# Kernel tuning notes

Measured on AMD Instinct MI355X. Metric: run time of the kernel, lower is better.

The kernel has to match this reference:

```python
import jax, jax.numpy as jnp
import numpy as np

ALPHA = 0.9
EPS = 1e-5
SEQ, BATCH, D_MODEL, FF_DIM = 2048, 16, 512, 2048


def _layer_norm(x, g, b):
    m = jnp.mean(x, axis=-1, keepdims=True)
    v = jnp.mean((x - m) ** 2, axis=-1, keepdims=True)
    return (x - m) * jax.lax.rsqrt(v + EPS) * g + b


def _decay_matrix(seq, dtype):
    # Closed form of the torch roll/flip/tril loop:
    #   W[i, j] = alpha^{i-j+1}            for j <= i
    #   W[i, i] += 1 - sum_{k=1}^{i+1} alpha^k   (diag correction)
    i = jnp.arange(seq)
    diff = i[:, None] - i[None, :]                       # [S, S]
    causal = diff >= 0
    expo = jnp.where(causal, diff + 1, 0).astype(dtype)
    W = jnp.where(causal, jnp.asarray(ALPHA, dtype) ** expo, 0.0)
    W = W + jnp.diag(1.0 - W.sum(axis=1))
    return W


def setup_inputs() -> dict:
    key = jax.random.key(0)
    ks = jax.random.split(key, 8)
    s = lambda fan: 1.0 / np.sqrt(fan)
    return {
        "x": jax.random.normal(ks[0], (SEQ, BATCH, D_MODEL), jnp.float32),
        "w_lin": jax.random.normal(ks[1], (D_MODEL, D_MODEL), jnp.float32) * s(D_MODEL),
        "b_lin": jax.random.normal(ks[2], (D_MODEL,), jnp.float32) * 0.01,
        "w1": jax.random.normal(ks[3], (FF_DIM, D_MODEL), jnp.float32) * s(D_MODEL),
        "b1": jax.random.normal(ks[4], (FF_DIM,), jnp.float32) * 0.01,
        "w2": jax.random.normal(ks[5], (D_MODEL, FF_DIM), jnp.float32) * s(FF_DIM),
        "b2": jax.random.normal(ks[6], (D_MODEL,), jnp.float32) * 0.01,
        "g1": jnp.ones((D_MODEL,), jnp.float32),
        "beta1": jnp.zeros((D_MODEL,), jnp.float32),
        "g2": jnp.ones((D_MODEL,), jnp.float32),
        "beta2": jnp.zeros((D_MODEL,), jnp.float32),
    }


def reference(x, w_lin, b_lin, w1, b1, w2, b2, g1, beta1, g2, beta2):
    seq = x.shape[0]
    W = _decay_matrix(seq, x.dtype)                      # [S, S]

    # attention sublayer (dropout = identity in eval)
    y = _layer_norm(x, g1, beta1)
    z = jnp.einsum("sbd,ed->sbe", y, w_lin) + b_lin       # projection
    attn = jnp.einsum("ih,hbd->ibd", W, z)                # causal exp-decay mixing
    x = x + attn

    # feed-forward sublayer
    y = _layer_norm(x, g2, beta2)
    h = jax.nn.relu(jnp.einsum("sbd,fd->sbf", y, w1) + b1)
    ff = jnp.einsum("sbf,df->sbd", h, w2) + b2
    return x + ff
```

## Files before the change

kernel.cpp:

```cpp
#include <hip/hip_runtime.h>

#define SEQ 2048
#define BATCH 16
#define DMODEL 512
#define FFDIM 2048
#define NTOK (SEQ * BATCH)
#define ALPHA 0.9f

typedef unsigned short u16;
typedef unsigned int u32;
typedef __attribute__((ext_vector_type(8))) short short8;
typedef __attribute__((ext_vector_type(4))) float f32x4;

__device__ __forceinline__ float bf2f(u16 u) {
    unsigned int v = ((unsigned int)u) << 16;
    return __builtin_bit_cast(float, v);
}
__device__ __forceinline__ u16 f2bf(float f) {
    unsigned int v = __builtin_bit_cast(unsigned int, f);
    v += 0x7fffu + ((v >> 16) & 1u);
    return (u16)(v >> 16);
}

__global__ __launch_bounds__(256) void cvt_kernel(const float* __restrict__ in,
                                                  u16* __restrict__ out, int n) {
    const int i = (blockIdx.x * 256 + threadIdx.x) * 4;
    if (i >= n) return;
    float4 v = *(const float4*)(in + i);
    ushort4 o;
    o.x = f2bf(v.x); o.y = f2bf(v.y); o.z = f2bf(v.z); o.w = f2bf(v.w);
    *(ushort4*)(out + i) = o;
}

__global__ __launch_bounds__(256) void ln_kernel(const float* __restrict__ xin,
                                                 const float* __restrict__ g,
                                                 const float* __restrict__ b,
                                                 u16* __restrict__ y) {
    const int lane = threadIdx.x & 63;
    const int wave = threadIdx.x >> 6;
    const long tok = (long)blockIdx.x * 4 + wave;
    const long off = tok * DMODEL + lane * 8;

    float f[8];
    {
        const float4* xp = (const float4*)(xin + off);
        float4 a = xp[0], c = xp[1];
        f[0] = a.x; f[1] = a.y; f[2] = a.z; f[3] = a.w;
        f[4] = c.x; f[5] = c.y; f[6] = c.z; f[7] = c.w;
    }
    float s = 0.f, s2 = 0.f;
#pragma unroll
    for (int i = 0; i < 8; i++) { s += f[i]; s2 += f[i] * f[i]; }
#pragma unroll
    for (int o = 32; o > 0; o >>= 1) {
        s += __shfl_xor(s, o, 64);
        s2 += __shfl_xor(s2, o, 64);
    }
    const float mean = s * (1.f / DMODEL);
    const float var = s2 * (1.f / DMODEL) - mean * mean;
    const float inv = rsqrtf(var + 1e-5f);

    const float4* gp = (const float4*)(g + lane * 8);
    const float4* bp = (const float4*)(b + lane * 8);
    float4 g0 = gp[0], g1 = gp[1], b0 = bp[0], b1 = bp[1];
    float gg[8] = {g0.x, g0.y, g0.z, g0.w, g1.x, g1.y, g1.z, g1.w};
    float bb[8] = {b0.x, b0.y, b0.z, b0.w, b1.x, b1.y, b1.z, b1.w};
    short8 ov;
#pragma unroll
    for (int i = 0; i < 8; i++)
        ov[i] = (short)f2bf((f[i] - mean) * inv * gg[i] + bb[i]);
    *(short8*)(y + off) = ov;
}

#define SCAN_L 64
#define SCAN_H 128
#define NCOLU (BATCH * DMODEL / 2)
__global__ __launch_bounds__(256) void scan_kernel(const u16* __restrict__ z,
                                                   const float* __restrict__ x,
                                                   float* __restrict__ x1) {
    const int colu = blockIdx.x * 256 + threadIdx.x;
    const int s0 = blockIdx.y * SCAN_L;

    const u32* zp = (const u32*)z;
    const float2* xp = (const float2*)x;
    float2* x1p = (float2*)x1;

    float r0 = 0.f, r1 = 0.f;

    {
        int sb = s0 - SCAN_H;
        if (sb < 0) sb = 0;
        const int nw = s0 - sb;
        if (nw > 0) {
            u32 zq[4];
#pragma unroll
            for (int j = 0; j < 4; j++) zq[j] = zp[(long)(sb + j) * NCOLU + colu];
            for (int i = 0; i < nw; i += 4) {
#pragma unroll
                for (int j = 0; j < 4; j++) {
                    const u32 zz = zq[j];
                    if (i + j + 4 < nw)
                        zq[j] = zp[(long)(sb + i + j + 4) * NCOLU + colu];
                    r0 = ALPHA * (bf2f((u16)(zz & 0xffffu)) + r0);
                    r1 = ALPHA * (bf2f((u16)(zz >> 16)) + r1);
                }
            }
        }
    }

    float ap = powf(ALPHA, (float)(s0 + 2));

    u32 zq[4];
    float2 xq[4];
#pragma unroll
    for (int j = 0; j < 4; j++) {
        zq[j] = zp[(long)(s0 + j) * NCOLU + colu];
        xq[j] = xp[(long)(s0 + j) * NCOLU + colu];
    }
#pragma unroll 4
    for (int i = 0; i < SCAN_L; i++) {
        const int sl = i & 3;
        const u32 zz = zq[sl];
        const float2 xx = xq[sl];
        if (i + 4 < SCAN_L) {
            zq[sl] = zp[(long)(s0 + i + 4) * NCOLU + colu];
            xq[sl] = xp[(long)(s0 + i + 4) * NCOLU + colu];
        }
        const float z0 = bf2f((u16)(zz & 0xffffu));
        const float z1 = bf2f((u16)(zz >> 16));
        r0 = ALPHA * (z0 + r0);
        r1 = ALPHA * (z1 + r1);
        const float c = 1.f - (ALPHA - ap) * 10.f;
        ap *= ALPHA;
        x1p[(long)(s0 + i) * NCOLU + colu] = (float2){xx.x + r0 + c * z0, xx.y + r1 + c * z1};
    }
}

#define BM 256
#define BN 256
#define BKK 64

typedef __attribute__((address_space(1))) unsigned int as1_u32;
typedef __attribute__((address_space(3))) unsigned int as3_u32;

__device__ __forceinline__ void gld_lds16(const void* g, const void* l) {
    __builtin_amdgcn_global_load_lds((as1_u32*)(unsigned long long)g,
                                     (as3_u32*)(unsigned int)(unsigned long long)l,
                                     16, 0, 0);
}

template <int EPI, bool OUT_F32>
__global__ __launch_bounds__(512, 2) void gemm8p(const u16* __restrict__ A,
                                                 const u16* __restrict__ Bt,
                                                 const float* __restrict__ bias,
                                                 const float* __restrict__ resid,
                                                 void* __restrict__ C,
                                                 int M, int N, int K) {
    __shared__ alignas(16) u16 sA[2][2][256 * 32];
    __shared__ alignas(16) u16 sB[2][2][256 * 32];

    const int tid = threadIdx.x;
    const int lane = tid & 63;
    const int wave = tid >> 6;
    const int wr = wave >> 2;
    const int wc = wave & 3;
    const int l15 = lane & 15, q16 = lane >> 4;

    const int gy = gridDim.y;
    const int nwg = gridDim.x * gy;
    const int d = blockIdx.y * gridDim.x + blockIdx.x;
    const int wgid = (d & 7) * (nwg >> 3) + (d >> 3);
    const int m0 = (wgid / gy) * BM;
    const int n0 = (wgid % gy) * BN;

    const u16* gA[2];
    const u16* gB[2];
    int dsto[2];
#pragma unroll
    for (int j = 0; j < 2; j++) {
        const int o = tid + j * 512;
        const int r = o >> 2;
        const int c = (o & 3) ^ ((o >> 3) & 3);
        gA[j] = A + (long)(m0 + r) * K + c * 8;
        gB[j] = Bt + (long)(n0 + r) * K + c * 8;
        dsto[j] = o * 8;
    }

    const int xoct = (q16 ^ ((l15 >> 1) & 3)) * 8;
    const int rowA = wr * 128 + l15;
    const int rowB = wc * 64 + l15;

    f32x4 acc[8][4];
#pragma unroll
    for (int i = 0; i < 8; i++)
#pragma unroll
        for (int j = 0; j < 4; j++) acc[i][j] = (f32x4){0.f, 0.f, 0.f, 0.f};

    const int NT = K / BKK;

#define STG_A(bs, kh, koff)                                                 \
    {                                                                       \
        gld_lds16(gA[0] + (koff) + (kh) * 32, &sA[bs][kh][dsto[0]]);        \
        gld_lds16(gA[1] + (koff) + (kh) * 32, &sA[bs][kh][dsto[1]]);        \
    }
#define STG_B(bs, kh, koff)                                                 \
    {                                                                       \
        gld_lds16(gB[0] + (koff) + (kh) * 32, &sB[bs][kh][dsto[0]]);        \
        gld_lds16(gB[1] + (koff) + (kh) * 32, &sB[bs][kh][dsto[1]]);        \
    }
#define MFMA16(mh)                                                          \
    {                                                                       \
        __builtin_amdgcn_s_setprio(1);                                      \
        _Pragma("unroll") for (int mi = 0; mi < 4; mi++)                    \
            _Pragma("unroll") for (int nj = 0; nj < 4; nj++)                \
                acc[(mh)*4 + mi][nj] = __builtin_amdgcn_mfma_f32_16x16x32_bf16( \
                    af[mi], bf[nj], acc[(mh)*4 + mi][nj], 0, 0, 0);         \
        __builtin_amdgcn_s_setprio(0);                                      \
    }
#define PHASE_END                                                           \
    {                                                                       \
        __builtin_amdgcn_sched_barrier(0);                                  \
        __builtin_amdgcn_s_barrier();                                       \
    }

    STG_A(0, 0, 0); STG_B(0, 0, 0); STG_A(0, 1, 0); STG_B(0, 1, 0);
    asm volatile("s_waitcnt vmcnt(4)" ::: "memory");
    __builtin_amdgcn_s_barrier();

#pragma unroll 1
    for (int t = 0; t < NT; ++t) {
        const int b = t & 1, bn = b ^ 1;
        const int ko = (t + 1) * BKK;
        const bool nx = (t + 1 < NT);
        short8 af[4], bf[4];

#pragma unroll
        for (int nj = 0; nj < 4; nj++)
            bf[nj] = *(const short8*)(&sB[b][0][(rowB + nj * 16) * 32 + xoct]);
#pragma unroll
        for (int mi = 0; mi < 4; mi++)
            af[mi] = *(const short8*)(&sA[b][0][(rowA + mi * 16) * 32 + xoct]);
        if (nx) STG_A(bn, 0, ko);
        MFMA16(0);
        PHASE_END;

#pragma unroll
        for (int mi = 0; mi < 4; mi++)
            af[mi] = *(const short8*)(&sA[b][0][(rowA + 64 + mi * 16) * 32 + xoct]);
        if (nx) STG_B(bn, 0, ko);
        MFMA16(1);
        if (nx) asm volatile("s_waitcnt vmcnt(4)" ::: "memory");
        else    asm volatile("s_waitcnt vmcnt(0)" ::: "memory");
        PHASE_END;

#pragma unroll
        for (int nj = 0; nj < 4; nj++)
            bf[nj] = *(const short8*)(&sB[b][1][(rowB + nj * 16) * 32 + xoct]);
#pragma unroll
        for (int mi = 0; mi < 4; mi++)
            af[mi] = *(const short8*)(&sA[b][1][(rowA + mi * 16) * 32 + xoct]);
        if (nx) STG_A(bn, 1, ko);
        MFMA16(0);
        PHASE_END;

#pragma unroll
        for (int mi = 0; mi < 4; mi++)
            af[mi] = *(const short8*)(&sA[b][1][(rowA + 64 + mi * 16) * 32 + xoct]);
        if (nx) STG_B(bn, 1, ko);
        MFMA16(1);
        if (nx) asm volatile("s_waitcnt vmcnt(4)" ::: "memory");
        else    asm volatile("s_waitcnt vmcnt(0)" ::: "memory");
        PHASE_END;
    }

#pragma unroll
    for (int mf = 0; mf < 8; mf++) {
        const int row0 = m0 + wr * 128 + mf * 16 + q16 * 4;
#pragma unroll
        for (int nj = 0; nj < 4; nj++) {
            const int col = n0 + wc * 64 + nj * 16 + l15;
            const float bv = bias[col];
#pragma unroll
            for (int r = 0; r < 4; r++) {
                const long idx = (long)(row0 + r) * N + col;
                float v = acc[mf][nj][r] + bv;
                if (EPI == 1) v = fmaxf(v, 0.f);
                if (EPI == 2) v += resid[idx];
                if (OUT_F32)
                    ((float*)C)[idx] = v;
                else
                    ((u16*)C)[idx] = f2bf(v);
            }
        }
    }
#undef STG_A
#undef STG_B
#undef MFMA16
#undef PHASE_END
}

extern "C" void kernel_launch(void* const* d_in, const int* in_sizes, int n_in,
                              void* d_out, int out_size, void* d_ws, size_t ws_size,
                              hipStream_t stream) {
    const float* x = (const float*)d_in[0];
    const float* w_lin = (const float*)d_in[1];
    const float* b_lin = (const float*)d_in[2];
    const float* w1 = (const float*)d_in[3];
    const float* b1 = (const float*)d_in[4];
    const float* w2 = (const float*)d_in[5];
    const float* b2 = (const float*)d_in[6];
    const float* g1 = (const float*)d_in[7];
    const float* be1 = (const float*)d_in[8];
    const float* g2 = (const float*)d_in[9];
    const float* be2 = (const float*)d_in[10];
    float* out = (float*)d_out;

    char* ws = (char*)d_ws;
    const size_t MB = 1024 * 1024;
    u16* y = (u16*)(ws);
    float* x1 = (float*)(ws + 32 * MB);
    u16* h = (u16*)(ws + 96 * MB);
    u16* z = h;
    u16* wb_lin = (u16*)(ws + 224 * MB);
    u16* wb1 = (u16*)(ws + 225 * MB);
    u16* wb2 = (u16*)(ws + 228 * MB);

    cvt_kernel<<<(DMODEL * DMODEL) / 1024, 256, 0, stream>>>(w_lin, wb_lin, DMODEL * DMODEL);
    cvt_kernel<<<(FFDIM * DMODEL) / 1024, 256, 0, stream>>>(w1, wb1, FFDIM * DMODEL);
    cvt_kernel<<<(DMODEL * FFDIM) / 1024, 256, 0, stream>>>(w2, wb2, DMODEL * FFDIM);

    ln_kernel<<<NTOK / 4, 256, 0, stream>>>(x, g1, be1, y);
    gemm8p<0, false><<<dim3(NTOK / BM, DMODEL / BN), 512, 0, stream>>>(y, wb_lin, b_lin, nullptr,
                                                                      z, NTOK, DMODEL, DMODEL);
    scan_kernel<<<dim3(NCOLU / 256, SEQ / SCAN_L), 256, 0, stream>>>(z, x, x1);
    ln_kernel<<<NTOK / 4, 256, 0, stream>>>(x1, g2, be2, y);
    gemm8p<1, false><<<dim3(NTOK / BM, FFDIM / BN), 512, 0, stream>>>(y, wb1, b1, nullptr, h,
                                                                     NTOK, FFDIM, DMODEL);
    gemm8p<2, true><<<dim3(NTOK / BM, DMODEL / BN), 512, 0, stream>>>(h, wb2, b2, x1, out,
                                                                     NTOK, DMODEL, FFDIM);
}
```

Measured before the change: 429.6 us.

## Replace truncated lookback scan with chunked three-pass decay scan with carries

```diff
diff --git a/kernel.cpp b/kernel.cpp
--- a/kernel.cpp
+++ b/kernel.cpp
@@ -73,40 +73,57 @@
 }
 
 #define SCAN_L 64
-#define SCAN_H 128
+#define NCHUNK (SEQ / SCAN_L)
 #define NCOLU (BATCH * DMODEL / 2)
+#define A64 1.17901846e-3f
+
+__global__ __launch_bounds__(256) void wsum_kernel(const u16* __restrict__ z,
+                                                   float* __restrict__ W) {
+    const int colu = blockIdx.x * 256 + threadIdx.x;
+    const int c = blockIdx.y;
+    const int sb = c * SCAN_L;
+    const u32* zp = (const u32*)z;
+
+    float w0 = 0.f, w1 = 0.f;
+    u32 zq[4];
+#pragma unroll
+    for (int j = 0; j < 4; j++) zq[j] = zp[(long)(sb + j) * NCOLU + colu];
+#pragma unroll 4
+    for (int i = 0; i < SCAN_L; i++) {
+        const int sl = i & 3;
+        const u32 zz = zq[sl];
+        if (i + 4 < SCAN_L) zq[sl] = zp[(long)(sb + i + 4) * NCOLU + colu];
+        w0 = ALPHA * (bf2f((u16)(zz & 0xffffu)) + w0);
+        w1 = ALPHA * (bf2f((u16)(zz >> 16)) + w1);
+    }
+    ((float2*)W)[(long)c * NCOLU + colu] = (float2){w0, w1};
+}
+
+__global__ __launch_bounds__(256) void carry_kernel(const float* __restrict__ W,
+                                                    float* __restrict__ R) {
+    const int col = blockIdx.x * 256 + threadIdx.x;
+    float r = 0.f;
+#pragma unroll
+    for (int c = 0; c < NCHUNK; c++) {
+        R[(long)c * 8192 + col] = r;
+        r = A64 * r + W[(long)c * 8192 + col];
+    }
+}
+
 __global__ __launch_bounds__(256) void scan_kernel(const u16* __restrict__ z,
                                                    const float* __restrict__ x,
+                                                   const float* __restrict__ Rbuf,
                                                    float* __restrict__ x1) {
     const int colu = blockIdx.x * 256 + threadIdx.x;
-    const int s0 = blockIdx.y * SCAN_L;
+    const int c = blockIdx.y;
+    const int s0 = c * SCAN_L;
 
     const u32* zp = (const u32*)z;
     const float2* xp = (const float2*)x;
     float2* x1p = (float2*)x1;
 
-    float r0 = 0.f, r1 = 0.f;
-
-    {
-        int sb = s0 - SCAN_H;
-        if (sb < 0) sb = 0;
-        const int nw = s0 - sb;
-        if (nw > 0) {
-            u32 zq[4];
-#pragma unroll
-            for (int j = 0; j < 4; j++) zq[j] = zp[(long)(sb + j) * NCOLU + colu];
-            for (int i = 0; i < nw; i += 4) {
-#pragma unroll
-                for (int j = 0; j < 4; j++) {
-                    const u32 zz = zq[j];
-                    if (i + j + 4 < nw)
-                        zq[j] = zp[(long)(sb + i + j + 4) * NCOLU + colu];
-                    r0 = ALPHA * (bf2f((u16)(zz & 0xffffu)) + r0);
-                    r1 = ALPHA * (bf2f((u16)(zz >> 16)) + r1);
-                }
-            }
-        }
-    }
+    const float2 rr = ((const float2*)Rbuf)[(long)c * NCOLU + colu];
+    float r0 = rr.x, r1 = rr.y;
 
     float ap = powf(ALPHA, (float)(s0 + 2));
 
@@ -130,9 +147,9 @@
         const float z1 = bf2f((u16)(zz >> 16));
         r0 = ALPHA * (z0 + r0);
         r1 = ALPHA * (z1 + r1);
-        const float c = 1.f - (ALPHA - ap) * 10.f;
+        const float cc = 1.f - (ALPHA - ap) * 10.f;
         ap *= ALPHA;
-        x1p[(long)(s0 + i) * NCOLU + colu] = (float2){xx.x + r0 + c * z0, xx.y + r1 + c * z1};
+        x1p[(long)(s0 + i) * NCOLU + colu] = (float2){xx.x + r0 + cc * z0, xx.y + r1 + cc * z1};
     }
 }
 
@@ -321,6 +338,8 @@
     float* x1 = (float*)(ws + 32 * MB);
     u16* h = (u16*)(ws + 96 * MB);
     u16* z = h;
+    float* Wbuf = (float*)(ws + 160 * MB);
+    float* Rbuf = (float*)(ws + 162 * MB);
     u16* wb_lin = (u16*)(ws + 224 * MB);
     u16* wb1 = (u16*)(ws + 225 * MB);
     u16* wb2 = (u16*)(ws + 228 * MB);
@@ -332,7 +351,9 @@
     ln_kernel<<<NTOK / 4, 256, 0, stream>>>(x, g1, be1, y);
     gemm8p<0, false><<<dim3(NTOK / BM, DMODEL / BN), 512, 0, stream>>>(y, wb_lin, b_lin, nullptr,
                                                                       z, NTOK, DMODEL, DMODEL);
-    scan_kernel<<<dim3(NCOLU / 256, SEQ / SCAN_L), 256, 0, stream>>>(z, x, x1);
+    wsum_kernel<<<dim3(NCOLU / 256, NCHUNK), 256, 0, stream>>>(z, Wbuf);
+    carry_kernel<<<8192 / 256, 256, 0, stream>>>(Wbuf, Rbuf);
+    scan_kernel<<<dim3(NCOLU / 256, NCHUNK), 256, 0, stream>>>(z, x, Rbuf, x1);
     ln_kernel<<<NTOK / 4, 256, 0, stream>>>(x1, g2, be2, y);
     gemm8p<1, false><<<dim3(NTOK / BM, FFDIM / BN), 512, 0, stream>>>(y, wb1, b1, nullptr, h,
                                                                      NTOK, FFDIM, DMODEL);
```

Measured after the change: 421.1 us. 2.0% less time.
